# Kernel tuning notes

Measured on AMD Instinct MI355X. Metric: run time of the kernel, lower is better.

The kernel has to match this reference:

```python
import jax, jax.numpy as jnp
import numpy as np

N_E = 50000
N_R = 1000
E = 800000
E_HIDDEN = 256
R_HIDDEN = 64
NEG_SLOPE = 0.01  # torch F.leaky_relu default


def segment_softmax(logits, seg, num_segments):
    # numerically stable per-segment softmax over edges
    seg_max = jax.ops.segment_max(logits, seg, num_segments=num_segments)
    seg_max = jnp.where(jnp.isfinite(seg_max), seg_max, 0.0)
    ex = jnp.exp(logits - seg_max[seg])
    denom = jax.ops.segment_sum(ex, seg, num_segments=num_segments)
    return ex / (denom[seg] + 1e-16)


def setup_inputs() -> dict:
    key = jax.random.key(0)
    ks = jax.random.split(key, 9)
    return {
        "x_e": jax.random.normal(ks[0], (N_E, E_HIDDEN), dtype=jnp.float32),
        "x_r": jax.random.normal(ks[1], (N_R, R_HIDDEN), dtype=jnp.float32),
        "edge_index": jax.random.randint(ks[2], (2, E), 0, N_E, dtype=jnp.int64),
        "rel": jax.random.randint(ks[3], (E,), 0, N_R, dtype=jnp.int64),
        "line_graph_index": jax.random.randint(ks[4], (2, E), 0, E, dtype=jnp.int64),
        "line_graph_val": jax.random.uniform(ks[5], (E,), dtype=jnp.float32),
        "a_h_w": jax.random.normal(ks[6], (E_HIDDEN,), dtype=jnp.float32),
        "a_t_w": jax.random.normal(ks[7], (E_HIDDEN,), dtype=jnp.float32),
        "a_r_w": jax.random.normal(ks[8], (R_HIDDEN,), dtype=jnp.float32),
    }


def reference(x_e, x_r, edge_index, rel, line_graph_index, line_graph_val, a_h_w, a_t_w, a_r_w):
    head, tail = edge_index[0], edge_index[1]
    # per-node scalar scores, gathered per edge
    s_e_h = jnp.einsum("nd,d->n", x_e, a_h_w)  # [N_e]
    s_e_t = jnp.einsum("nd,d->n", x_e, a_t_w)  # [N_e]
    s_r = jnp.einsum("rd,d->r", x_r, a_r_w)    # [N_r]
    e_h = s_e_h[head]
    e_t = s_e_t[tail]
    e_r = s_r[rel]

    n_e = x_e.shape[0]
    msg = x_r[rel]  # [E, r_hidden]

    # head branch: segment softmax over head groups, scatter-aggregate x_r[rel]
    alpha_h = segment_softmax(jax.nn.leaky_relu(e_h + e_r, NEG_SLOPE), head, n_e)
    x_e_h = jax.ops.segment_sum(alpha_h[:, None] * msg, head, num_segments=n_e)

    # tail branch: softmax grouped by tail, but spmm still scatters into head rows
    alpha_t = segment_softmax(jax.nn.leaky_relu(e_t + e_r, NEG_SLOPE), tail, n_e)
    x_e_t = jax.ops.segment_sum(alpha_t[:, None] * msg, tail, num_segments=n_e)

    return jnp.concatenate([x_e_h, x_e_t], axis=1)  # [N_e, 2*r_hidden]
```

## Files before the change

kernel.cpp:

```cpp
#include <hip/hip_runtime.h>

static constexpr int kNE = 50000;
static constexpr int kNR = 1000;
static constexpr int kE  = 800000;
static constexpr int kEH = 256;
static constexpr int kRH = 64;
static constexpr float kNeg = 0.01f;

static constexpr int kSegsPerB = 64;
static constexpr int kSegs = 2 * kNE;
static constexpr int kB = (kSegs + kSegsPerB - 1) / kSegsPerB;
static constexpr int kCap = 1536;
static constexpr int kEdgesPerBin = 2048;
static constexpr int kChunkRecs  = 2 * kEdgesPerBin;
static constexpr int kBinBlocks  = (kE + kEdgesPerBin - 1) / kEdgesPerBin;
static constexpr int kTabCols    = 392;
static constexpr int kNodeBlocks = kNE / 8;
static constexpr int kRelBlocks  = kNR / 8;
static constexpr int kCntPad = 2048;

__device__ __forceinline__ float lrelu(float x){ return x > 0.f ? x : kNeg * x; }

__global__ __launch_bounds__(512) void k_bin_scores(
        const float* __restrict__ xe, const float* __restrict__ ahw,
        const float* __restrict__ atw, const float* __restrict__ xr,
        const float* __restrict__ arw,
        const int* __restrict__ head, const int* __restrict__ tail,
        const int* __restrict__ rel,
        float* __restrict__ s_h, float* __restrict__ s_t, float* __restrict__ s_r,
        unsigned short* __restrict__ chunk, unsigned short* __restrict__ tab){
    __shared__ int cnt[kCntPad];
    __shared__ int cur[kCntPad];
    __shared__ unsigned int srt[kChunkRecs];
    __shared__ int wsum[8];

    int blk = blockIdx.x;
    int tid = threadIdx.x;
    int lane = tid & 63;

    if (blk >= kBinBlocks){
        int sb = blk - kBinBlocks;
        if (sb < kNodeBlocks){
            int node = sb * 8 + (tid >> 6);
            const float4* row = (const float4*)(xe + (size_t)node * kEH);
            float4 xv = row[lane];
            float4 av = ((const float4*)ahw)[lane];
            float4 bv = ((const float4*)atw)[lane];
            float ph = xv.x*av.x + xv.y*av.y + xv.z*av.z + xv.w*av.w;
            float pt = xv.x*bv.x + xv.y*bv.y + xv.z*bv.z + xv.w*bv.w;
            #pragma unroll
            for (int o = 32; o > 0; o >>= 1){
                ph += __shfl_down(ph, o, 64);
                pt += __shfl_down(pt, o, 64);
            }
            if (lane == 0){ s_h[node] = ph; s_t[node] = pt; }
        } else {
            int r = (sb - kNodeBlocks) * 8 + (tid >> 6);
            float p = xr[(size_t)r * kRH + lane] * arw[lane];
            #pragma unroll
            for (int o = 32; o > 0; o >>= 1) p += __shfl_down(p, o, 64);
            if (lane == 0) s_r[r] = p;
        }
        return;
    }

    int e0 = blk * kEdgesPerBin;
    for (int i = tid; i < kCntPad; i += 512) cnt[i] = 0;
    __syncthreads();

    unsigned int recs[8];
    unsigned short rnk[8];
    #pragma unroll
    for (int p = 0; p < 4; ++p){
        int e = e0 + p * 512 + tid;
        unsigned int rh = 0xFFFFFFFFu, rt = 0xFFFFFFFFu;
        unsigned short kh = 0, kt = 0;
        if (e < kE){
            int h = head[e], t = tail[e], r = rel[e];
            rh = ((unsigned int)h << 10) | (unsigned int)r;
            rt = ((unsigned int)(kNE + t) << 10) | (unsigned int)r;
            kh = (unsigned short)atomicAdd(&cnt[rh >> 16], 1);
            kt = (unsigned short)atomicAdd(&cnt[rt >> 16], 1);
        }
        recs[p] = rh; recs[4 + p] = rt;
        rnk[p]  = kh; rnk[4 + p]  = kt;
    }
    __syncthreads();

    int c0 = cnt[4 * tid], c1 = cnt[4 * tid + 1], c2 = cnt[4 * tid + 2], c3 = cnt[4 * tid + 3];
    int v = c0 + c1 + c2 + c3;
    int x = v;
    #pragma unroll
    for (int o = 1; o < 64; o <<= 1){
        int y = __shfl_up(x, o, 64);
        if (lane >= o) x += y;
    }
    int wv = tid >> 6;
    if (lane == 63) wsum[wv] = x;
    __syncthreads();
    int wpre = 0, tot = 0;
    #pragma unroll
    for (int w = 0; w < 8; ++w){
        int s = wsum[w];
        if (w < wv) wpre += s;
        tot += s;
    }
    int base = wpre + x - v;
    cur[4 * tid]     = base;
    cur[4 * tid + 1] = base + c0;
    cur[4 * tid + 2] = base + c0 + c1;
    cur[4 * tid + 3] = base + c0 + c1 + c2;
    __syncthreads();

    #pragma unroll
    for (int p = 0; p < 8; ++p){
        unsigned int rc = recs[p];
        if (rc != 0xFFFFFFFFu){
            int slot = cur[rc >> 16] + (int)rnk[p];
            srt[slot] = rc;
        }
    }
    __syncthreads();

    unsigned int* cw = (unsigned int*)(chunk + (size_t)blk * kChunkRecs);
    for (int j2 = tid; j2 < (tot >> 1); j2 += 512){
        unsigned int lo = srt[2 * j2] & 0xFFFFu;
        unsigned int hi = srt[2 * j2 + 1] & 0xFFFFu;
        cw[j2] = lo | (hi << 16);
    }
    for (int i = tid; i < kB; i += 512)
        tab[(size_t)i * kTabCols + blk] = (unsigned short)cur[i];
    if (tid == 0)
        tab[(size_t)kB * kTabCols + blk] = (unsigned short)tot;
}

__global__ __launch_bounds__(256) void k_sort_aggregate(
        const unsigned short* __restrict__ chunk, const unsigned short* __restrict__ tab,
        const float* __restrict__ s_h, const float* __restrict__ s_t,
        const float* __restrict__ s_r, const float* __restrict__ xr,
        float* __restrict__ out){
    __shared__ float srl[kNR];
    __shared__ float sn[kSegsPerB];
    __shared__ unsigned short arr[kCap];
    __shared__ unsigned short relbuf[kCap];
    __shared__ float alphabuf[kCap];
    __shared__ int cnt[kSegsPerB], start[kSegsPerB];
    __shared__ unsigned int mx[kSegsPerB];
    __shared__ unsigned short order[kSegsPerB];
    __shared__ int gsum[4];

    int b = blockIdx.x;
    int tid = threadIdx.x;
    int lane = tid & 63;
    int wv = tid >> 6;

    for (int i = tid; i < kNR; i += 256) srl[i] = s_r[i];
    if (tid < kSegsPerB){
        cnt[tid] = 0;
        mx[tid] = 0u;
        int gseg = b * kSegsPerB + tid;
        float s = 0.f;
        if (gseg < kNE) s = s_h[gseg];
        else if (gseg < kSegs) s = s_t[gseg - kNE];
        sn[tid] = s;
    }
    __syncthreads();

    const unsigned short* rowS = tab + (size_t)b * kTabCols;
    const unsigned short* rowE = tab + (size_t)(b + 1) * kTabCols;
    int nrec = 0;
    for (int c0 = 0; c0 < kBinBlocks; c0 += 256){
        int c = c0 + tid;
        int s = 0, L = 0;
        if (c < kBinBlocks){
            s = rowS[c];
            L = (int)rowE[c] - s;
        }
        int x = L;
        #pragma unroll
        for (int o = 1; o < 64; o <<= 1){
            int y = __shfl_up(x, o, 64);
            if (lane >= o) x += y;
        }
        if (lane == 63) gsum[wv] = x;
        __syncthreads();
        int wpre = 0, stot = 0;
        #pragma unroll
        for (int w = 0; w < 4; ++w){
            int g = gsum[w];
            if (w < wv) wpre += g;
            stot += g;
        }
        int off = nrec + wpre + x - L;
        if (off + L > kCap) L = max(0, kCap - off);
        const unsigned short* src = chunk + (size_t)c * kChunkRecs + s;
        for (int i = 0; i < L; ++i) arr[off + i] = src[i];
        nrec += stot;
        __syncthreads();
    }
    if (nrec > kCap) nrec = kCap;

    unsigned short recs[6], rnk[6];
    #pragma unroll
    for (int p = 0; p < 6; ++p){
        int idx = p * 256 + tid;
        unsigned short rc = 0xFFFFu, rk = 0;
        if (idx < nrec){
            rc = arr[idx];
            rk = (unsigned short)atomicAdd(&cnt[rc >> 10], 1);
        }
        recs[p] = rc; rnk[p] = rk;
    }
    __syncthreads();
    if (tid < kSegsPerB){
        int c = cnt[tid];
        int x = c;
        #pragma unroll
        for (int o = 1; o < 64; o <<= 1){
            int y = __shfl_up(x, o, 64);
            if (tid >= o) x += y;
        }
        start[tid] = x - c;

        unsigned int key = ((unsigned int)c << 6) | (unsigned int)tid;
        #pragma unroll
        for (int k = 2; k <= 64; k <<= 1){
            #pragma unroll
            for (int j = k >> 1; j > 0; j >>= 1){
                unsigned int o2 = __shfl_xor(key, j, 64);
                bool keepMin = (((tid & j) == 0) == ((tid & k) == 0));
                unsigned int mn = key < o2 ? key : o2;
                unsigned int mxk = key < o2 ? o2 : key;
                key = keepMin ? mn : mxk;
            }
        }
        order[tid] = (unsigned short)(key & 63u);
    }
    __syncthreads();
    #pragma unroll
    for (int p = 0; p < 6; ++p){
        unsigned short rc = recs[p];
        if (rc != 0xFFFFu){
            int ls = rc >> 10;
            int rr = rc & 1023;
            int slot = start[ls] + (int)rnk[p];
            float lg = lrelu(sn[ls] + srl[rr]);
            unsigned int s32 = __float_as_uint(lg);
            unsigned int key = (s32 & 0x80000000u) ? ~s32 : (s32 | 0x80000000u);
            atomicMax(&mx[ls], key);
            relbuf[slot] = (unsigned short)rr;
            alphabuf[slot] = lg;
        }
    }
    __syncthreads();

    int grp = tid >> 4;
    int sub = tid & 15;
    #pragma unroll
    for (int i = 0; i < 4; ++i){
        int ls = order[i * 16 + grp];
        int gseg = b * kSegsPerB + ls;
        if (gseg >= kSegs) continue;
        int deg = cnt[ls], st = start[ls];

        unsigned int u = mx[ls];
        float m = __uint_as_float((u & 0x80000000u) ? (u & 0x7FFFFFFFu) : ~u);

        float ss = 0.f;
        for (int k = sub; k < deg; k += 16){
            float e = __expf(alphabuf[st + k] - m);
            alphabuf[st + k] = e;
            ss += e;
        }
        #pragma unroll
        for (int o = 1; o < 16; o <<= 1) ss += __shfl_xor(ss, o, 64);
        float inv = 1.f / (ss + 1e-16f);

        float4 acc = {0.f, 0.f, 0.f, 0.f};
        int k = 0;
        for (; k + 4 <= deg; k += 4){
            int r0 = relbuf[st + k],     r1 = relbuf[st + k + 1];
            int r2 = relbuf[st + k + 2], r3 = relbuf[st + k + 3];
            float a0 = alphabuf[st + k],     a1 = alphabuf[st + k + 1];
            float a2 = alphabuf[st + k + 2], a3 = alphabuf[st + k + 3];
            float4 v0 = ((const float4*)(xr + (size_t)r0 * kRH))[sub];
            float4 v1 = ((const float4*)(xr + (size_t)r1 * kRH))[sub];
            float4 v2 = ((const float4*)(xr + (size_t)r2 * kRH))[sub];
            float4 v3 = ((const float4*)(xr + (size_t)r3 * kRH))[sub];
            acc.x += a0*v0.x + a1*v1.x + a2*v2.x + a3*v3.x;
            acc.y += a0*v0.y + a1*v1.y + a2*v2.y + a3*v3.y;
            acc.z += a0*v0.z + a1*v1.z + a2*v2.z + a3*v3.z;
            acc.w += a0*v0.w + a1*v1.w + a2*v2.w + a3*v3.w;
        }
        for (; k < deg; ++k){
            int rr = relbuf[st + k];
            float a = alphabuf[st + k];
            float4 v = ((const float4*)(xr + (size_t)rr * kRH))[sub];
            acc.x += a*v.x; acc.y += a*v.y; acc.z += a*v.z; acc.w += a*v.w;
        }
        acc.x *= inv; acc.y *= inv; acc.z *= inv; acc.w *= inv;

        bool isHead = gseg < kNE;
        int node = isHead ? gseg : gseg - kNE;
        float4* op = (float4*)(out + (size_t)node * (2 * kRH) + (isHead ? 0 : kRH));
        op[sub] = acc;
    }
}

extern "C" void kernel_launch(void* const* d_in, const int* in_sizes, int n_in,
                              void* d_out, int out_size, void* d_ws, size_t ws_size,
                              hipStream_t stream) {
    const float* xe  = (const float*)d_in[0];
    const float* xr  = (const float*)d_in[1];
    const int* edge_index = (const int*)d_in[2];
    const int* rel        = (const int*)d_in[3];
    const float* ahw = (const float*)d_in[6];
    const float* atw = (const float*)d_in[7];
    const float* arw = (const float*)d_in[8];
    float* out = (float*)d_out;

    const int* head = edge_index;
    const int* tail = edge_index + kE;

    char* ws = (char*)d_ws;
    float* s_h  = (float*)ws;                    ws += kNE * sizeof(float);
    float* s_t  = (float*)ws;                    ws += kNE * sizeof(float);
    float* s_r  = (float*)ws;                    ws += ((kNR + 256) & ~255) * sizeof(float);
    unsigned short* chunk = (unsigned short*)ws; ws += (size_t)kBinBlocks * kChunkRecs * sizeof(unsigned short);
    unsigned short* tab   = (unsigned short*)ws; ws += (size_t)(kB + 1) * kTabCols * sizeof(unsigned short);

    k_bin_scores<<<kBinBlocks + kNodeBlocks + kRelBlocks, 512, 0, stream>>>(
        xe, ahw, atw, xr, arw, head, tail, rel, s_h, s_t, s_r, chunk, tab);
    k_sort_aggregate<<<kB, 256, 0, stream>>>(chunk, tab, s_h, s_t, s_r, xr, out);
}
```

Measured before the change: 149.0 us.

## Transpose offset table and replace serial chunk copy with binary-search gather

The bin offset table is now stored row-major per bin block, so each binning block writes a contiguous row instead of scattered strided stores. The aggregate kernel no longer copies each chunk's records serially into a shared staging array. It builds a prefix-sum table of offsets per source chunk and has each thread binary-search it to fetch its record straight from global memory. This removes the per-thread serial copy loop and its load imbalance, at the cost of an extra binary search per record and scattered 2-byte global loads instead of coalesced reads.

New measurement: 145.5 us (median of 2 runs). 1.02x faster.

```diff
diff --git a/kernel.cpp b/kernel.cpp
--- a/kernel.cpp
+++ b/kernel.cpp
@@ -14,7 +14,7 @@
 static constexpr int kEdgesPerBin = 2048;
 static constexpr int kChunkRecs  = 2 * kEdgesPerBin;
 static constexpr int kBinBlocks  = (kE + kEdgesPerBin - 1) / kEdgesPerBin;
-static constexpr int kTabCols    = 392;
+static constexpr int kTabW       = kB + 1;
 static constexpr int kNodeBlocks = kNE / 8;
 static constexpr int kRelBlocks  = kNR / 8;
 static constexpr int kCntPad = 2048;
@@ -128,10 +128,9 @@
         unsigned int hi = srt[2 * j2 + 1] & 0xFFFFu;
         cw[j2] = lo | (hi << 16);
     }
-    for (int i = tid; i < kB; i += 512)
-        tab[(size_t)i * kTabCols + blk] = (unsigned short)cur[i];
-    if (tid == 0)
-        tab[(size_t)kB * kTabCols + blk] = (unsigned short)tot;
+    unsigned short* trow = tab + (size_t)blk * kTabW;
+    for (int i = tid; i < kB; i += 512) trow[i] = (unsigned short)cur[i];
+    if (tid == 0) trow[kB] = (unsigned short)tot;
 }
 
 __global__ __launch_bounds__(256) void k_sort_aggregate(
@@ -141,9 +140,10 @@
         float* __restrict__ out){
     __shared__ float srl[kNR];
     __shared__ float sn[kSegsPerB];
-    __shared__ unsigned short arr[kCap];
     __shared__ unsigned short relbuf[kCap];
     __shared__ float alphabuf[kCap];
+    __shared__ int cumOff[kBinBlocks + 1];
+    __shared__ int srcBase[kBinBlocks];
     __shared__ int cnt[kSegsPerB], start[kSegsPerB];
     __shared__ unsigned int mx[kSegsPerB];
     __shared__ unsigned short order[kSegsPerB];
@@ -164,17 +164,18 @@
         else if (gseg < kSegs) s = s_t[gseg - kNE];
         sn[tid] = s;
     }
-    __syncthreads();
-
-    const unsigned short* rowS = tab + (size_t)b * kTabCols;
-    const unsigned short* rowE = tab + (size_t)(b + 1) * kTabCols;
-    int nrec = 0;
+    if (tid == 0) cumOff[0] = 0;
+    __syncthreads();
+
+    int nrecBase = 0;
     for (int c0 = 0; c0 < kBinBlocks; c0 += 256){
         int c = c0 + tid;
-        int s = 0, L = 0;
+        int L = 0;
         if (c < kBinBlocks){
-            s = rowS[c];
-            L = (int)rowE[c] - s;
+            const unsigned short* trow = tab + (size_t)c * kTabW;
+            int s = trow[b];
+            L = (int)trow[b + 1] - s;
+            srcBase[c] = c * kChunkRecs + s;
         }
         int x = L;
         #pragma unroll
@@ -191,22 +192,25 @@
             if (w < wv) wpre += g;
             stot += g;
         }
-        int off = nrec + wpre + x - L;
-        if (off + L > kCap) L = max(0, kCap - off);
-        const unsigned short* src = chunk + (size_t)c * kChunkRecs + s;
-        for (int i = 0; i < L; ++i) arr[off + i] = src[i];
-        nrec += stot;
+        if (c < kBinBlocks) cumOff[c + 1] = nrecBase + wpre + x;
+        nrecBase += stot;
         __syncthreads();
     }
-    if (nrec > kCap) nrec = kCap;
+    int nrec = nrecBase > kCap ? kCap : nrecBase;
 
     unsigned short recs[6], rnk[6];
     #pragma unroll
     for (int p = 0; p < 6; ++p){
-        int idx = p * 256 + tid;
+        int j = p * 256 + tid;
         unsigned short rc = 0xFFFFu, rk = 0;
-        if (idx < nrec){
-            rc = arr[idx];
+        if (j < nrec){
+            int lo = 0, hi = kBinBlocks;
+            #pragma unroll 1
+            while (hi - lo > 1){
+                int mid = (lo + hi) >> 1;
+                if (cumOff[mid] <= j) lo = mid; else hi = mid;
+            }
+            rc = chunk[srcBase[lo] + (j - cumOff[lo])];
             rk = (unsigned short)atomicAdd(&cnt[rc >> 10], 1);
         }
         recs[p] = rc; rnk[p] = rk;
@@ -327,7 +331,7 @@
     float* s_t  = (float*)ws;                    ws += kNE * sizeof(float);
     float* s_r  = (float*)ws;                    ws += ((kNR + 256) & ~255) * sizeof(float);
     unsigned short* chunk = (unsigned short*)ws; ws += (size_t)kBinBlocks * kChunkRecs * sizeof(unsigned short);
-    unsigned short* tab   = (unsigned short*)ws; ws += (size_t)(kB + 1) * kTabCols * sizeof(unsigned short);
+    unsigned short* tab   = (unsigned short*)ws; ws += (size_t)kBinBlocks * kTabW * sizeof(unsigned short);
 
     k_bin_scores<<<kBinBlocks + kNodeBlocks + kRelBlocks, 512, 0, stream>>>(
         xe, ahw, atw, xr, arw, head, tail, rel, s_h, s_t, s_r, chunk, tab);
```
